# Performance work log

Measured on AMD Instinct MI355X. Metric: run time of the kernel, lower is better.

The kernel has to match this reference:

```python
import jax, jax.numpy as jnp
import numpy as np

D_MODEL = 2048
N_HEADS = 16
D_K = D_MODEL // N_HEADS
NB_FEAT = 8  # ceil(ln(2048))
BLOCK_H = 1
BLOCK_W = 1
EPS = 1e-6


def setup_inputs() -> dict:
    key = jax.random.key(0)
    ks = jax.random.split(key, 8)
    B, S = 2, 4096
    q = jax.random.normal(ks[0], (B, S, D_MODEL), dtype=jnp.float32)
    k = jax.random.normal(ks[1], (B, S, D_MODEL), dtype=jnp.float32)
    v = jax.random.normal(ks[2], (B, S, D_MODEL), dtype=jnp.float32)
    # torch Linear weights [out, in]
    w_q = jax.random.normal(ks[3], (D_MODEL, D_MODEL), dtype=jnp.float32) / np.sqrt(D_MODEL)
    w_k = jax.random.normal(ks[4], (D_MODEL, D_MODEL), dtype=jnp.float32) / np.sqrt(D_MODEL)
    w_v = jax.random.normal(ks[5], (D_MODEL, D_MODEL), dtype=jnp.float32) / np.sqrt(D_MODEL)
    w_o = jax.random.normal(ks[6], (D_MODEL, D_MODEL), dtype=jnp.float32) / np.sqrt(D_MODEL)
    omega = jax.random.normal(ks[7], (NB_FEAT, D_K), dtype=jnp.float32) / np.sqrt(D_K)
    return {"q": q, "k": k, "v": v, "w_q": w_q, "w_k": w_k, "w_v": w_v, "w_o": w_o, "omega": omega}


def _kernel(x):
    # kernel_type == 'exp'
    return jnp.exp(-0.5 * x * x)


def reference(q, k, v, w_q, w_k, w_v, w_o, omega):
    B, Sq, D = q.shape
    Sk = k.shape[1]
    # projections (torch Linear: x @ W.T), split heads -> [B, S, H, d_k]
    qh = (q @ w_q.T).reshape(B, Sq, N_HEADS, D_K)
    kh = (k @ w_k.T).reshape(B, Sk, N_HEADS, D_K)
    vh = (v @ w_v.T).reshape(B, Sk, N_HEADS, D_K)
    # random-feature maps -> [B, S, H, nb]
    q_prime = _kernel(jnp.einsum('bshd,nd->bshn', qh, omega))
    k_prime = _kernel(jnp.einsum('bshd,nd->bshn', kh, omega))
    q_prime = q_prime / (q_prime.sum(-1, keepdims=True) + EPS)
    k_prime = k_prime / (k_prime.sum(-1, keepdims=True) + EPS)
    # causal prefix sums along sequence
    K_cum = jnp.cumsum(k_prime, axis=1)                                   # [B,S,H,nb]
    KV_cum = jnp.cumsum(k_prime[..., None] * vh[..., None, :], axis=1)    # [B,S,H,nb,d_k]
    # blockwise causal key selection
    q_idx = jnp.arange(Sq)
    key_idx = jnp.minimum((q_idx // BLOCK_H + 1) * BLOCK_W - 1, Sk - 1)   # [Sq]
    K_sel = K_cum[:, key_idx]    # [B,Sq,H,nb]
    KV_sel = KV_cum[:, key_idx]  # [B,Sq,H,nb,d_k]
    numerator = jnp.einsum('bshn,bshnd->bshd', q_prime, KV_sel)
    denominator = jnp.sum(q_prime * K_sel, axis=-1, keepdims=True)
    out = numerator / (denominator + EPS)
    out = out.reshape(B, Sq, D)
    return out @ w_o.T
```

## Files before the change

kernel.cpp:

```cpp
#include <hip/hip_runtime.h>
#include <hip/hip_bf16.h>
#include <cstdint>

#define B_SZ 2
#define S_LEN 4096
#define R_TOT 8192
#define DM 2048
#define NH 16
#define DK 128
#define NFEAT 8
#define CHUNK 128
#define NCHUNK 32
#define KSPL 512
#define EPSF 1e-6f

typedef short bf16x8_t __attribute__((ext_vector_type(8)));
typedef float f32x4_t __attribute__((ext_vector_type(4)));

__device__ __forceinline__ ushort f2bf(float f) {
  uint32_t u = __float_as_uint(f);
  u += 0x7FFF + ((u >> 16) & 1);
  return (ushort)(u >> 16);
}
__device__ __forceinline__ float bf2f(ushort u) {
  return __uint_as_float(((uint32_t)u) << 16);
}

__global__ __launch_bounds__(256) void cast_f32_bf16(const float* __restrict__ src,
                                                     ushort* __restrict__ dst, int n4) {
  int i = blockIdx.x * 256 + threadIdx.x;
  if (i >= n4) return;
  float4 f = reinterpret_cast<const float4*>(src)[i];
  ushort4 o;
  o.x = f2bf(f.x); o.y = f2bf(f.y); o.z = f2bf(f.z); o.w = f2bf(f.w);
  reinterpret_cast<ushort4*>(dst)[i] = o;
}

__global__ __launch_bounds__(256) void fold_kernel(const float* __restrict__ W,
                                                   const float* __restrict__ omega,
                                                   ushort* __restrict__ O) {
  __shared__ float som[NFEAT * DK];
  const int h = blockIdx.y;
  const int j = blockIdx.x * 256 + threadIdx.x;
  for (int i = threadIdx.x; i < NFEAT * DK; i += 256) som[i] = omega[i];
  __syncthreads();
  float acc[NFEAT] = {0.f, 0.f, 0.f, 0.f, 0.f, 0.f, 0.f, 0.f};
  for (int d = 0; d < DK; d++) {
    const float w = W[(size_t)(h * DK + d) * DM + j];
#pragma unroll
    for (int n = 0; n < NFEAT; n++) acc[n] += w * som[n * DK + d];
  }
#pragma unroll
  for (int n = 0; n < NFEAT; n++) O[(size_t)(h * NFEAT + n) * DM + j] = f2bf(acc[n]);
}

#define MFMA_BLK(mb, A0_, A1_, A2_, A3_, B0_, B1_, B2_, B3_)                                  \
  acc[mb + 0][0] = __builtin_amdgcn_mfma_f32_16x16x32_bf16(A0_, B0_, acc[mb + 0][0], 0, 0, 0); \
  acc[mb + 1][0] = __builtin_amdgcn_mfma_f32_16x16x32_bf16(A1_, B0_, acc[mb + 1][0], 0, 0, 0); \
  acc[mb + 2][0] = __builtin_amdgcn_mfma_f32_16x16x32_bf16(A2_, B0_, acc[mb + 2][0], 0, 0, 0); \
  acc[mb + 3][0] = __builtin_amdgcn_mfma_f32_16x16x32_bf16(A3_, B0_, acc[mb + 3][0], 0, 0, 0); \
  acc[mb + 0][1] = __builtin_amdgcn_mfma_f32_16x16x32_bf16(A0_, B1_, acc[mb + 0][1], 0, 0, 0); \
  acc[mb + 1][1] = __builtin_amdgcn_mfma_f32_16x16x32_bf16(A1_, B1_, acc[mb + 1][1], 0, 0, 0); \
  acc[mb + 2][1] = __builtin_amdgcn_mfma_f32_16x16x32_bf16(A2_, B1_, acc[mb + 2][1], 0, 0, 0); \
  acc[mb + 3][1] = __builtin_amdgcn_mfma_f32_16x16x32_bf16(A3_, B1_, acc[mb + 3][1], 0, 0, 0); \
  acc[mb + 0][2] = __builtin_amdgcn_mfma_f32_16x16x32_bf16(A0_, B2_, acc[mb + 0][2], 0, 0, 0); \
  acc[mb + 1][2] = __builtin_amdgcn_mfma_f32_16x16x32_bf16(A1_, B2_, acc[mb + 1][2], 0, 0, 0); \
  acc[mb + 2][2] = __builtin_amdgcn_mfma_f32_16x16x32_bf16(A2_, B2_, acc[mb + 2][2], 0, 0, 0); \
  acc[mb + 3][2] = __builtin_amdgcn_mfma_f32_16x16x32_bf16(A3_, B2_, acc[mb + 3][2], 0, 0, 0); \
  acc[mb + 0][3] = __builtin_amdgcn_mfma_f32_16x16x32_bf16(A0_, B3_, acc[mb + 0][3], 0, 0, 0); \
  acc[mb + 1][3] = __builtin_amdgcn_mfma_f32_16x16x32_bf16(A1_, B3_, acc[mb + 1][3], 0, 0, 0); \
  acc[mb + 2][3] = __builtin_amdgcn_mfma_f32_16x16x32_bf16(A2_, B3_, acc[mb + 2][3], 0, 0, 0); \
  acc[mb + 3][3] = __builtin_amdgcn_mfma_f32_16x16x32_bf16(A3_, B3_, acc[mb + 3][3], 0, 0, 0);

template<int BF16OUT>
__global__ __launch_bounds__(512, 1) void gemm256(const ushort* __restrict__ A,
                                                  const ushort* __restrict__ Bm,
                                                  void* __restrict__ Cv,
                                                  int M, int N, int K) {
  __shared__ ushort lds[8 * 8192];
  const int tid = threadIdx.x;
  const int wave = tid >> 6, lane = tid & 63;
  const int wm = wave >> 2, wn = wave & 3;
  const int NKT = K >> 6;

  const int nb = N >> 8;
  const int cpx = gridDim.x >> 3;
  const int swz = (blockIdx.x & 7) * cpx + (blockIdx.x >> 3);
  const int bx = swz % nb, by = swz / nb;
  const int m0 = by * 256, n0 = bx * 256;

  auto stage = [&](int bufi, int ab, int kh, int kt, const ushort* G, int r0) {
    ushort* Lr = lds + (((bufi << 1) | ab) << 1 | kh) * 8192;
#pragma unroll
    for (int j = 0; j < 2; j++) {
      const int c = j * 512 + wave * 64 + lane;
      const int row = c >> 2, slot = c & 3;
      const int ss = slot ^ ((row >> 1) & 3);
      const ushort* g = G + (size_t)(r0 + row) * K + kt * 64 + kh * 32 + ss * 8;
      __builtin_amdgcn_global_load_lds(
          (const __attribute__((address_space(1))) void*)g,
          (__attribute__((address_space(3))) void*)(Lr + (j * 512 + wave * 64) * 8), 16, 0, 0);
    }
  };
  auto rdA = [&](int bufi, int kh, int m) -> bf16x8_t {
    const int row = wm * 128 + m * 16 + (lane & 15);
    const int slot = (lane >> 4) ^ ((row >> 1) & 3);
    return *reinterpret_cast<const bf16x8_t*>(lds + ((bufi << 2) | kh) * 8192 + row * 32 + slot * 8);
  };
  auto rdB = [&](int bufi, int kh, int nf) -> bf16x8_t {
    const int row = wn * 64 + nf * 16 + (lane & 15);
    const int slot = (lane >> 4) ^ ((row >> 1) & 3);
    return *reinterpret_cast<const bf16x8_t*>(lds + (((bufi << 1) | 1) << 1 | kh) * 8192 + row * 32 + slot * 8);
  };

  f32x4_t acc[8][4];
#pragma unroll
  for (int m = 0; m < 8; m++)
#pragma unroll
    for (int nf = 0; nf < 4; nf++) acc[m][nf] = (f32x4_t){0.f, 0.f, 0.f, 0.f};

  stage(0, 0, 0, 0, A, m0);  stage(0, 1, 0, 0, Bm, n0);
  stage(0, 0, 1, 0, A, m0);  stage(0, 1, 1, 0, Bm, n0);
  stage(1, 0, 0, 1, A, m0);  stage(1, 1, 0, 1, Bm, n0);
  asm volatile("s_waitcnt vmcnt(8)" ::: "memory");
  __builtin_amdgcn_s_barrier();
  __builtin_amdgcn_sched_barrier(0);

  bf16x8_t pA0 = rdA(0, 0, 0), pA1 = rdA(0, 0, 1), pA2 = rdA(0, 0, 2), pA3 = rdA(0, 0, 3);
  bf16x8_t B00 = rdB(0, 0, 0), B01 = rdB(0, 0, 1), B02 = rdB(0, 0, 2), B03 = rdB(0, 0, 3);
  bf16x8_t qA0, qA1, qA2, qA3, B10, B11, B12, B13;

  for (int t = 0; t < NKT; t++) {
    const int buf = t & 1;
    const int t1 = (t + 1 < NKT) ? t + 1 : NKT - 1;
    const int t2 = (t + 2 < NKT) ? t + 2 : NKT - 1;

    qA0 = rdA(buf, 0, 4); qA1 = rdA(buf, 0, 5); qA2 = rdA(buf, 0, 6); qA3 = rdA(buf, 0, 7);
    stage(buf ^ 1, 0, 1, t1, A, m0);
    __builtin_amdgcn_s_setprio(1);
    MFMA_BLK(0, pA0, pA1, pA2, pA3, B00, B01, B02, B03)
    __builtin_amdgcn_s_setprio(0);
    asm volatile("s_waitcnt vmcnt(6)" ::: "memory");
    __builtin_amdgcn_s_barrier();
    __builtin_amdgcn_sched_barrier(0);

    pA0 = rdA(buf, 1, 0); pA1 = rdA(buf, 1, 1); pA2 = rdA(buf, 1, 2); pA3 = rdA(buf, 1, 3);
    B10 = rdB(buf, 1, 0); B11 = rdB(buf, 1, 1); B12 = rdB(buf, 1, 2); B13 = rdB(buf, 1, 3);
    stage(buf ^ 1, 1, 1, t1, Bm, n0);
    __builtin_amdgcn_s_setprio(1);
    MFMA_BLK(4, qA0, qA1, qA2, qA3, B00, B01, B02, B03)
    __builtin_amdgcn_s_setprio(0);
    __builtin_amdgcn_s_barrier();
    __builtin_amdgcn_sched_barrier(0);

    qA0 = rdA(buf, 1, 4); qA1 = rdA(buf, 1, 5); qA2 = rdA(buf, 1, 6); qA3 = rdA(buf, 1, 7);
    stage(buf, 0, 0, t2, A, m0);
    __builtin_amdgcn_s_setprio(1);
    MFMA_BLK(0, pA0, pA1, pA2, pA3, B10, B11, B12, B13)
    __builtin_amdgcn_s_setprio(0);
    asm volatile("s_waitcnt vmcnt(6)" ::: "memory");
    __builtin_amdgcn_s_barrier();
    __builtin_amdgcn_sched_barrier(0);

    pA0 = rdA(buf ^ 1, 0, 0); pA1 = rdA(buf ^ 1, 0, 1); pA2 = rdA(buf ^ 1, 0, 2); pA3 = rdA(buf ^ 1, 0, 3);
    B00 = rdB(buf ^ 1, 0, 0); B01 = rdB(buf ^ 1, 0, 1); B02 = rdB(buf ^ 1, 0, 2); B03 = rdB(buf ^ 1, 0, 3);
    stage(buf, 1, 0, t2, Bm, n0);
    __builtin_amdgcn_s_setprio(1);
    MFMA_BLK(4, qA0, qA1, qA2, qA3, B10, B11, B12, B13)
    __builtin_amdgcn_s_setprio(0);
    __builtin_amdgcn_s_barrier();
    __builtin_amdgcn_sched_barrier(0);
  }
  asm volatile("s_waitcnt vmcnt(0)" ::: "memory");

#pragma unroll
  for (int m = 0; m < 8; m++) {
    const int rb = m0 + wm * 128 + m * 16 + (lane >> 4) * 4;
#pragma unroll
    for (int nf = 0; nf < 4; nf++) {
      const int col = n0 + wn * 64 + nf * 16 + (lane & 15);
#pragma unroll
      for (int r = 0; r < 4; r++) {
        const float val = acc[m][nf][r];
        if (BF16OUT)
          ((ushort*)Cv)[(size_t)(rb + r) * N + col] = f2bf(val);
        else
          ((float*)Cv)[(size_t)(rb + r) * N + col] = val;
      }
    }
  }
}

__global__ __launch_bounds__(256) void gemm_thin(const ushort* __restrict__ A,
                                                 const ushort* __restrict__ Bm,
                                                 float* __restrict__ P,
                                                 int M, int K) {
  __shared__ ushort lds_a[128 * 32];
  __shared__ ushort lds_b[128 * 32];
  const int t = threadIdx.x;
  const int wave = t >> 6, lane = t & 63;
  const int spl = blockIdx.x;
  const int m0 = blockIdx.y * 128;
  const int kb = spl * KSPL;
  const int wm = wave >> 1, wn = wave & 1;

  f32x4_t acc[4][4];
#pragma unroll
  for (int i = 0; i < 4; i++)
#pragma unroll
    for (int j = 0; j < 4; j++) acc[i][j] = (f32x4_t){0.f, 0.f, 0.f, 0.f};

  const int srow = lane >> 2;
  const int skoff = (lane & 3) * 8;

  for (int k0 = kb; k0 < kb + KSPL; k0 += 32) {
#pragma unroll
    for (int i = 0; i < 2; i++) {
      const int rgrp = i * 4 + wave;
      const int row = rgrp * 16 + srow;
      const ushort* ga = A + (size_t)(m0 + row) * K + (k0 + skoff);
      const ushort* gb = Bm + (size_t)row * K + (k0 + skoff);
      __builtin_amdgcn_global_load_lds(
          (const __attribute__((address_space(1))) void*)ga,
          (__attribute__((address_space(3))) void*)(lds_a + rgrp * 512), 16, 0, 0);
      __builtin_amdgcn_global_load_lds(
          (const __attribute__((address_space(1))) void*)gb,
          (__attribute__((address_space(3))) void*)(lds_b + rgrp * 512), 16, 0, 0);
    }
    __syncthreads();
    bf16x8_t af[4], bfr[4];
#pragma unroll
    for (int i = 0; i < 4; i++) {
      af[i]  = *reinterpret_cast<const bf16x8_t*>(
          lds_a + (wm * 64 + i * 16 + (lane & 15)) * 32 + (lane >> 4) * 8);
      bfr[i] = *reinterpret_cast<const bf16x8_t*>(
          lds_b + (wn * 64 + i * 16 + (lane & 15)) * 32 + (lane >> 4) * 8);
    }
#pragma unroll
    for (int i = 0; i < 4; i++)
#pragma unroll
      for (int j = 0; j < 4; j++)
        acc[i][j] = __builtin_amdgcn_mfma_f32_16x16x32_bf16(af[i], bfr[j], acc[i][j], 0, 0, 0);
    __syncthreads();
  }

  float* Pp = P + (size_t)spl * ((size_t)R_TOT * 128);
#pragma unroll
  for (int i = 0; i < 4; i++) {
    const int rb = m0 + wm * 64 + i * 16 + (lane >> 4) * 4;
#pragma unroll
    for (int j = 0; j < 4; j++) {
      const int col = wn * 64 + j * 16 + (lane & 15);
#pragma unroll
      for (int r = 0; r < 4; r++)
        Pp[(size_t)(rb + r) * 128 + col] = acc[i][j][r];
    }
  }
}

__global__ __launch_bounds__(256) void feat2_kernel(const float* __restrict__ P,
                                                    float* __restrict__ F) {
  const int g = blockIdx.x * 256 + threadIdx.x;
  const int row = g >> 4, h = g & 15;
  float4 a = {0.f, 0.f, 0.f, 0.f}, c = {0.f, 0.f, 0.f, 0.f};
#pragma unroll
  for (int s = 0; s < 4; s++) {
    const float4* xp = reinterpret_cast<const float4*>(
        P + (size_t)s * ((size_t)R_TOT * 128) + (size_t)row * 128 + h * NFEAT);
    const float4 u = xp[0], w = xp[1];
    a.x += u.x; a.y += u.y; a.z += u.z; a.w += u.w;
    c.x += w.x; c.y += w.y; c.z += w.z; c.w += w.w;
  }
  float x[8] = {a.x, a.y, a.z, a.w, c.x, c.y, c.z, c.w};
  float f[8], s = 0.f;
#pragma unroll
  for (int n = 0; n < 8; n++) { f[n] = __expf(-0.5f * x[n] * x[n]); s += f[n]; }
  const float inv = 1.f / (s + EPSF);
  const int b = row >> 12, sidx = row & 4095;
  float* out = F + ((size_t)(h * 2 + b) * 4096 + sidx) * 8;
  float4 o0 = {f[0] * inv, f[1] * inv, f[2] * inv, f[3] * inv};
  float4 o1 = {f[4] * inv, f[5] * inv, f[6] * inv, f[7] * inv};
  reinterpret_cast<float4*>(out)[0] = o0;
  reinterpret_cast<float4*>(out)[1] = o1;
}

__global__ __launch_bounds__(128) void chunk_sum_kernel(const float* __restrict__ KF,
                                                        const ushort* __restrict__ VH,
                                                        float* __restrict__ CKV,
                                                        float* __restrict__ CK) {
  const int cid = blockIdx.x;
  const int c = cid & 31, bh = cid >> 5, b = bh >> 4, h = bh & 15;
  const int d = threadIdx.x;
  __shared__ float s_kf[CHUNK * 8];
  const size_t fbase = ((size_t)(h * 2 + b) * 4096 + (size_t)c * CHUNK) * 8;
  {
    float4 a0 = *reinterpret_cast<const float4*>(KF + fbase + d * 8);
    float4 a1 = *reinterpret_cast<const float4*>(KF + fbase + d * 8 + 4);
    *reinterpret_cast<float4*>(s_kf + d * 8) = a0;
    *reinterpret_cast<float4*>(s_kf + d * 8 + 4) = a1;
  }
  __syncthreads();
  float kv[8] = {0, 0, 0, 0, 0, 0, 0, 0};
  float ks = 0.f;
  const ushort* vp = VH + ((size_t)b * S_LEN + (size_t)c * CHUNK) * DM + h * DK + d;
  for (int s = 0; s < CHUNK; s++) {
    const float v = bf2f(vp[(size_t)s * DM]);
#pragma unroll
    for (int n = 0; n < 8; n++) kv[n] += s_kf[s * 8 + n] * v;
    ks += s_kf[s * 8 + (d & 7)];
  }
#pragma unroll
  for (int n = 0; n < 8; n++) CKV[((size_t)cid * 8 + n) * 128 + d] = kv[n];
  if (d < 8) CK[cid * 8 + d] = ks;
}

__global__ __launch_bounds__(128) void chunk_scan2(float* __restrict__ CKV,
                                                   float* __restrict__ CK) {
  const int bh = blockIdx.x >> 3, n = blockIdx.x & 7;
  const int d = threadIdx.x;
  float v[NCHUNK];
#pragma unroll
  for (int c = 0; c < NCHUNK; c++)
    v[c] = CKV[((size_t)(bh * NCHUNK + c) * 8 + n) * 128 + d];
  float run = 0.f;
#pragma unroll
  for (int c = 0; c < NCHUNK; c++) {
    const float tv = v[c];
    CKV[((size_t)(bh * NCHUNK + c) * 8 + n) * 128 + d] = run;
    run += tv;
  }
  if (d < 32) {
    const int i = (bh * NCHUNK + d) * 8 + n;
    const float orig = CK[i];
    float inc = orig;
#pragma unroll
    for (int off = 1; off < 32; off <<= 1) {
      const float o = __shfl_up(inc, off, 32);
      if (d >= off) inc += o;
    }
    CK[i] = inc - orig;
  }
}

__global__ __launch_bounds__(128) void attn_scan_kernel(const float* __restrict__ QF,
                                                        const float* __restrict__ KF,
                                                        const ushort* __restrict__ VH,
                                                        const float* __restrict__ CKV,
                                                        const float* __restrict__ CK,
                                                        ushort* __restrict__ AO) {
  const int cid = blockIdx.x;
  const int c = cid & 31, bh = cid >> 5, b = bh >> 4, h = bh & 15;
  const int d = threadIdx.x;
  __shared__ float s_qf[CHUNK * 8];
  __shared__ float s_kf[CHUNK * 8];
  const size_t fbase = ((size_t)(h * 2 + b) * 4096 + (size_t)c * CHUNK) * 8;
  {
    float4 a0 = *reinterpret_cast<const float4*>(QF + fbase + d * 8);
    float4 a1 = *reinterpret_cast<const float4*>(QF + fbase + d * 8 + 4);
    float4 b0 = *reinterpret_cast<const float4*>(KF + fbase + d * 8);
    float4 b1 = *reinterpret_cast<const float4*>(KF + fbase + d * 8 + 4);
    *reinterpret_cast<float4*>(s_qf + d * 8) = a0;
    *reinterpret_cast<float4*>(s_qf + d * 8 + 4) = a1;
    *reinterpret_cast<float4*>(s_kf + d * 8) = b0;
    *reinterpret_cast<float4*>(s_kf + d * 8 + 4) = b1;
  }
  float kv[8], krun[8];
#pragma unroll
  for (int n = 0; n < 8; n++) kv[n] = CKV[((size_t)cid * 8 + n) * 128 + d];
#pragma unroll
  for (int n = 0; n < 8; n++) krun[n] = CK[cid * 8 + n];
  __syncthreads();
  const size_t row0 = (size_t)b * S_LEN + (size_t)c * CHUNK;
  const ushort* vp = VH + row0 * DM + h * DK + d;
  ushort* op = AO + row0 * DM + h * DK + d;
  for (int s = 0; s < CHUNK; s++) {
    const float v = bf2f(vp[(size_t)s * DM]);
    float num = 0.f, den = 0.f;
#pragma unroll
    for (int n = 0; n < 8; n++) {
      const float kf = s_kf[s * 8 + n];
      kv[n] += kf * v;
      krun[n] += kf;
      const float qf = s_qf[s * 8 + n];
      num += qf * kv[n];
      den += qf * krun[n];
    }
    op[(size_t)s * DM] = f2bf(num / (den + EPSF));
  }
}

extern "C" void kernel_launch(void* const* d_in, const int* in_sizes, int n_in,
                              void* d_out, int out_size, void* d_ws, size_t ws_size,
                              hipStream_t stream) {
  const float* q     = (const float*)d_in[0];
  const float* k     = (const float*)d_in[1];
  const float* v     = (const float*)d_in[2];
  const float* w_q   = (const float*)d_in[3];
  const float* w_k   = (const float*)d_in[4];
  const float* w_v   = (const float*)d_in[5];
  const float* w_o   = (const float*)d_in[6];
  const float* omega = (const float*)d_in[7];

  char* ws = (char*)d_ws;
  const size_t DD2 = (size_t)DM * DM * 2;
  const size_t OD2 = (size_t)NH * NFEAT * DM * 2;
  const size_t RD2 = (size_t)R_TOT * DM * 2;
  const size_t X4  = (size_t)R_TOT * NH * NFEAT * 4;

  ushort* wvb = (ushort*)(ws);
  ushort* wob = (ushort*)(ws + DD2);
  ushort* oqb = (ushort*)(ws + 2 * DD2);
  ushort* okb = (ushort*)(ws + 2 * DD2 + OD2);
  ushort* xb  = (ushort*)(ws + 2 * DD2 + 2 * OD2);
  ushort* vhb = (ushort*)(ws + 2 * DD2 + 2 * OD2 + RD2);
  float*  xp4 = (float*) (ws + 2 * DD2 + 2 * OD2 + RD2);
  float*  qf  = (float*) (ws + 2 * DD2 + 2 * OD2 + 2 * RD2);
  float*  kf  = (float*) (ws + 2 * DD2 + 2 * OD2 + 2 * RD2 + X4);
  float*  ckv = (float*) (ws + 2 * DD2 + 2 * OD2 + 2 * RD2 + 2 * X4);
  float*  ck  = (float*) (ws + 2 * DD2 + 2 * OD2 + 2 * RD2 + 3 * X4);
  ushort* ao  = xb;

  const int n4_in = R_TOT * DM / 4;
  const int n4_w  = DM * DM / 4;

  cast_f32_bf16<<<dim3(n4_w / 256), 256, 0, stream>>>(w_v, wvb, n4_w);
  cast_f32_bf16<<<dim3(n4_w / 256), 256, 0, stream>>>(w_o, wob, n4_w);
  fold_kernel<<<dim3(DM / 256, NH), 256, 0, stream>>>(w_q, omega, oqb);
  fold_kernel<<<dim3(DM / 256, NH), 256, 0, stream>>>(w_k, omega, okb);

  dim3 gg_thin(DM / KSPL, R_TOT / 128);

  cast_f32_bf16<<<dim3(n4_in / 256), 256, 0, stream>>>(q, xb, n4_in);
  gemm_thin<<<gg_thin, 256, 0, stream>>>(xb, oqb, xp4, R_TOT, DM);
  feat2_kernel<<<dim3(R_TOT * NH / 256), 256, 0, stream>>>(xp4, qf);

  cast_f32_bf16<<<dim3(n4_in / 256), 256, 0, stream>>>(k, xb, n4_in);
  gemm_thin<<<gg_thin, 256, 0, stream>>>(xb, okb, xp4, R_TOT, DM);
  feat2_kernel<<<dim3(R_TOT * NH / 256), 256, 0, stream>>>(xp4, kf);

  cast_f32_bf16<<<dim3(n4_in / 256), 256, 0, stream>>>(v, xb, n4_in);
  gemm256<1><<<dim3((R_TOT / 256) * (DM / 256)), 512, 0, stream>>>(xb, wvb, (void*)vhb, R_TOT, DM, DM);

  chunk_sum_kernel<<<dim3(B_SZ * NH * NCHUNK), 128, 0, stream>>>(kf, vhb, ckv, ck);
  chunk_scan2<<<dim3(B_SZ * NH * 8), 128, 0, stream>>>(ckv, ck);
  attn_scan_kernel<<<dim3(B_SZ * NH * NCHUNK), 128, 0, stream>>>(qf, kf, vhb, ckv, ck, ao);

  gemm256<0><<<dim3((R_TOT / 256) * (DM / 256)), 512, 0, stream>>>(ao, wob, d_out, R_TOT, DM, DM);
}
```

Before: 343.9 us.

## Fuse q/k bf16 cast into thin GEMM and batch paired launches

The thin q/k projection GEMM now reads fp32 activations directly, converts them to bf16 in registers and writes them to LDS. This removes the separate cast kernels and their bf16 round trip through memory. The q and k paths, plus the weight cast and fold kernels, are merged into single launches using an extra grid dimension, which cuts launch count and widens each grid. In exchange, the A-tile load becomes a synchronous register path instead of async global-to-LDS, doubling A bytes read per tile. The partial-sum buffer also doubles to hold both q and k.

```diff
diff --git a/kernel.cpp b/kernel.cpp
--- a/kernel.cpp
+++ b/kernel.cpp
@@ -36,10 +36,28 @@
   reinterpret_cast<ushort4*>(dst)[i] = o;
 }
 
-__global__ __launch_bounds__(256) void fold_kernel(const float* __restrict__ W,
-                                                   const float* __restrict__ omega,
-                                                   ushort* __restrict__ O) {
+__global__ __launch_bounds__(256) void wcast2(const float* __restrict__ w_v,
+                                              const float* __restrict__ w_o,
+                                              ushort* __restrict__ wvb,
+                                              ushort* __restrict__ wob, int n4) {
+  const float* src = blockIdx.y ? w_o : w_v;
+  ushort* dst = blockIdx.y ? wob : wvb;
+  int i = blockIdx.x * 256 + threadIdx.x;
+  if (i >= n4) return;
+  float4 f = reinterpret_cast<const float4*>(src)[i];
+  ushort4 o;
+  o.x = f2bf(f.x); o.y = f2bf(f.y); o.z = f2bf(f.z); o.w = f2bf(f.w);
+  reinterpret_cast<ushort4*>(dst)[i] = o;
+}
+
+__global__ __launch_bounds__(256) void fold2(const float* __restrict__ w_q,
+                                             const float* __restrict__ w_k,
+                                             const float* __restrict__ omega,
+                                             ushort* __restrict__ oqb,
+                                             ushort* __restrict__ okb) {
   __shared__ float som[NFEAT * DK];
+  const float* W = blockIdx.z ? w_k : w_q;
+  ushort* O = blockIdx.z ? okb : oqb;
   const int h = blockIdx.y;
   const int j = blockIdx.x * 256 + threadIdx.x;
   for (int i = threadIdx.x; i < NFEAT * DK; i += 256) som[i] = omega[i];
@@ -191,12 +209,16 @@
   }
 }
 
-__global__ __launch_bounds__(256) void gemm_thin(const ushort* __restrict__ A,
-                                                 const ushort* __restrict__ Bm,
-                                                 float* __restrict__ P,
-                                                 int M, int K) {
+__global__ __launch_bounds__(256) void gemm_thin2(const float* __restrict__ qin,
+                                                  const float* __restrict__ kin,
+                                                  const ushort* __restrict__ oqb,
+                                                  const ushort* __restrict__ okb,
+                                                  float* __restrict__ P) {
   __shared__ ushort lds_a[128 * 32];
   __shared__ ushort lds_b[128 * 32];
+  const int which = blockIdx.z;
+  const float* A = which ? kin : qin;
+  const ushort* Bm = which ? okb : oqb;
   const int t = threadIdx.x;
   const int wave = t >> 6, lane = t & 63;
   const int spl = blockIdx.x;
@@ -215,14 +237,21 @@
 
   for (int k0 = kb; k0 < kb + KSPL; k0 += 32) {
 #pragma unroll
+    for (int j = 0; j < 2; j++) {
+      const int g = j * 256 + t;
+      const int row = g >> 2, slot = g & 3;
+      const float4* gp = reinterpret_cast<const float4*>(A + (size_t)(m0 + row) * DM + k0 + slot * 8);
+      const float4 f0 = gp[0], f1 = gp[1];
+      union { ushort u[8]; bf16x8_t v; } pk;
+      pk.u[0] = f2bf(f0.x); pk.u[1] = f2bf(f0.y); pk.u[2] = f2bf(f0.z); pk.u[3] = f2bf(f0.w);
+      pk.u[4] = f2bf(f1.x); pk.u[5] = f2bf(f1.y); pk.u[6] = f2bf(f1.z); pk.u[7] = f2bf(f1.w);
+      *reinterpret_cast<bf16x8_t*>(lds_a + row * 32 + slot * 8) = pk.v;
+    }
+#pragma unroll
     for (int i = 0; i < 2; i++) {
       const int rgrp = i * 4 + wave;
       const int row = rgrp * 16 + srow;
-      const ushort* ga = A + (size_t)(m0 + row) * K + (k0 + skoff);
-      const ushort* gb = Bm + (size_t)row * K + (k0 + skoff);
-      __builtin_amdgcn_global_load_lds(
-          (const __attribute__((address_space(1))) void*)ga,
-          (__attribute__((address_space(3))) void*)(lds_a + rgrp * 512), 16, 0, 0);
+      const ushort* gb = Bm + (size_t)row * DM + (k0 + skoff);
       __builtin_amdgcn_global_load_lds(
           (const __attribute__((address_space(1))) void*)gb,
           (__attribute__((address_space(3))) void*)(lds_b + rgrp * 512), 16, 0, 0);
@@ -244,7 +273,7 @@
     __syncthreads();
   }
 
-  float* Pp = P + (size_t)spl * ((size_t)R_TOT * 128);
+  float* Pp = P + (size_t)which * (4ull * R_TOT * 128) + (size_t)spl * ((size_t)R_TOT * 128);
 #pragma unroll
   for (int i = 0; i < 4; i++) {
     const int rb = m0 + wm * 64 + i * 16 + (lane >> 4) * 4;
@@ -258,15 +287,19 @@
   }
 }
 
-__global__ __launch_bounds__(256) void feat2_kernel(const float* __restrict__ P,
-                                                    float* __restrict__ F) {
+__global__ __launch_bounds__(256) void feat2x2(const float* __restrict__ P,
+                                               float* __restrict__ qf,
+                                               float* __restrict__ kf) {
+  const int which = blockIdx.y;
+  const float* Pb = P + (size_t)which * (4ull * R_TOT * 128);
+  float* F = which ? kf : qf;
   const int g = blockIdx.x * 256 + threadIdx.x;
   const int row = g >> 4, h = g & 15;
   float4 a = {0.f, 0.f, 0.f, 0.f}, c = {0.f, 0.f, 0.f, 0.f};
 #pragma unroll
   for (int s = 0; s < 4; s++) {
     const float4* xp = reinterpret_cast<const float4*>(
-        P + (size_t)s * ((size_t)R_TOT * 128) + (size_t)row * 128 + h * NFEAT);
+        Pb + (size_t)s * ((size_t)R_TOT * 128) + (size_t)row * 128 + h * NFEAT);
     const float4 u = xp[0], w = xp[1];
     a.x += u.x; a.y += u.y; a.z += u.z; a.w += u.w;
     c.x += w.x; c.y += w.y; c.z += w.z; c.w += w.w;
@@ -423,20 +456,11 @@
   const int n4_in = R_TOT * DM / 4;
   const int n4_w  = DM * DM / 4;
 
-  cast_f32_bf16<<<dim3(n4_w / 256), 256, 0, stream>>>(w_v, wvb, n4_w);
-  cast_f32_bf16<<<dim3(n4_w / 256), 256, 0, stream>>>(w_o, wob, n4_w);
-  fold_kernel<<<dim3(DM / 256, NH), 256, 0, stream>>>(w_q, omega, oqb);
-  fold_kernel<<<dim3(DM / 256, NH), 256, 0, stream>>>(w_k, omega, okb);
-
-  dim3 gg_thin(DM / KSPL, R_TOT / 128);
-
-  cast_f32_bf16<<<dim3(n4_in / 256), 256, 0, stream>>>(q, xb, n4_in);
-  gemm_thin<<<gg_thin, 256, 0, stream>>>(xb, oqb, xp4, R_TOT, DM);
-  feat2_kernel<<<dim3(R_TOT * NH / 256), 256, 0, stream>>>(xp4, qf);
-
-  cast_f32_bf16<<<dim3(n4_in / 256), 256, 0, stream>>>(k, xb, n4_in);
-  gemm_thin<<<gg_thin, 256, 0, stream>>>(xb, okb, xp4, R_TOT, DM);
-  feat2_kernel<<<dim3(R_TOT * NH / 256), 256, 0, stream>>>(xp4, kf);
+  wcast2<<<dim3(n4_w / 256, 2), 256, 0, stream>>>(w_v, w_o, wvb, wob, n4_w);
+  fold2<<<dim3(DM / 256, NH, 2), 256, 0, stream>>>(w_q, w_k, omega, oqb, okb);
+
+  gemm_thin2<<<dim3(DM / KSPL, R_TOT / 128, 2), 256, 0, stream>>>(q, k, oqb, okb, xp4);
+  feat2x2<<<dim3(R_TOT * NH / 256, 2), 256, 0, stream>>>(xp4, qf, kf);
 
   cast_f32_bf16<<<dim3(n4_in / 256), 256, 0, stream>>>(v, xb, n4_in);
   gemm256<1><<<dim3((R_TOT / 256) * (DM / 256)), 512, 0, stream>>>(xb, wvb, (void*)vhb, R_TOT, DM, DM);
```

After: 292.8 us. -14.9%, faster.
